# Performance work log

Measured on AMD Instinct MI355X. Metric: run time of the kernel, lower is better.

Reference implementation:

```python
import jax, jax.numpy as jnp
import numpy as np

NEG_SLOPE = 0.2  # negative_slope of LeakyReLU in GATConv
N_NODES = 50000
N_EDGES = 800000
R = 2
IN_DIM = 128
HID = 32
HEADS = 4
OUT = 32


def setup_inputs() -> dict:
    key = jax.random.key(0)
    ks = jax.random.split(key, 12)
    s = 0.1  # keep pre-activations tame
    x = jax.random.normal(ks[0], (N_NODES, IN_DIM), dtype=jnp.float32)
    W1 = jax.random.normal(ks[1], (R, IN_DIM, HEADS * HID), dtype=jnp.float32) * s
    al1 = jax.random.normal(ks[2], (R, HEADS, HID), dtype=jnp.float32) * s
    ar1 = jax.random.normal(ks[3], (R, HEADS, HID), dtype=jnp.float32) * s
    b1 = jax.random.normal(ks[4], (R, HEADS * HID), dtype=jnp.float32) * s
    W2 = jax.random.normal(ks[5], (R, HEADS * HID, HEADS * OUT), dtype=jnp.float32) * s
    al2 = jax.random.normal(ks[6], (R, HEADS, OUT), dtype=jnp.float32) * s
    ar2 = jax.random.normal(ks[7], (R, HEADS, OUT), dtype=jnp.float32) * s
    b2 = jax.random.normal(ks[8], (R, HEADS * OUT), dtype=jnp.float32) * s
    edges = jax.random.randint(ks[9], (R, 2, N_EDGES), 0, N_NODES, dtype=jnp.int32)
    return {"x": x, "W1": W1, "al1": al1, "ar1": ar1, "b1": b1,
            "W2": W2, "al2": al2, "ar2": ar2, "b2": b2, "edges": edges}


def _gat_rel(h, W, al, ar, src, dst, n):
    """Single-relation GATConv aggregation (no bias/residual/activation)."""
    H, D = al.shape
    feat = (h @ W).reshape(n, H, D)                   # [N,H,D]
    el = jnp.einsum('nhd,hd->nh', feat, al)           # [N,H]
    er = jnp.einsum('nhd,hd->nh', feat, ar)
    e = el[src] + er[dst]                             # [E,H]
    e = jnp.where(e > 0, e, NEG_SLOPE * e)            # LeakyReLU
    # edge softmax over incoming edges of each dst node (numerically stable)
    m = jax.ops.segment_max(e, dst, num_segments=n)
    ex = jnp.exp(e - m[dst])
    denom = jax.ops.segment_sum(ex, dst, num_segments=n)
    alpha = ex / jnp.maximum(denom[dst], 1e-9)        # [E,H]
    msg = alpha[:, :, None] * feat[src]               # [E,H,D]
    return jax.ops.segment_sum(msg, dst, num_segments=n)  # [N,H,D]


def reference(x, W1, al1, ar1, b1, W2, al2, ar2, b2, edges):
    n = x.shape[0]
    r_count = edges.shape[0]
    H1, D1 = al1.shape[1:]
    # --- layer 1: per-relation GATConv (bias + elu inside), sum across relations
    acc = jnp.zeros((n, H1, D1), dtype=x.dtype)
    for r in range(r_count):
        src, dst = edges[r, 0], edges[r, 1]
        o = _gat_rel(x, W1[r], al1[r], ar1[r], src, dst, n)
        acc = acc + jax.nn.elu(o + b1[r].reshape(1, H1, D1))
    h = acc.reshape(n, H1 * D1)                       # flatten heads
    # --- layer 2: residual (identity, since in == heads*out), bias, no activation
    H2, D2 = al2.shape[1:]
    res = h.reshape(n, H2, D2)
    acc2 = jnp.zeros((n, H2, D2), dtype=x.dtype)
    for r in range(r_count):
        src, dst = edges[r, 0], edges[r, 1]
        o = _gat_rel(h, W2[r], al2[r], ar2[r], src, dst, n)
        acc2 = acc2 + o + res + b2[r].reshape(1, H2, D2)
    return acc2.mean(axis=1)                          # mean over heads -> [N, OUT]
```

## Files before the change

### kernel.cpp

```cpp
#include <hip/hip_runtime.h>
#include <math.h>

#define HEADS 4
#define DIM 32
#define FDIM 128
#define EPB 8192
#define BPBSH 8
#define WB 16

typedef __attribute__((ext_vector_type(8))) short short8;
typedef __attribute__((ext_vector_type(16))) float float16;

__device__ __forceinline__ unsigned short f2bf(float x) {
  unsigned u = __float_as_uint(x);
  u += 0x7FFFu + ((u >> 16) & 1);
  return (unsigned short)(u >> 16);
}

__global__ __launch_bounds__(256) void binA_kernel(const int* __restrict__ edges,
    int* __restrict__ cntA, const float* __restrict__ W1, const float* __restrict__ W2,
    unsigned short* __restrict__ WT, int E, int BA, int BAp, int R) {
  int r = blockIdx.y, blk = blockIdx.x, t = threadIdx.x;
  if (blk >= BA) {
    int wb = blk - BA;
    int base = wb * (32768 / WB);
#pragma unroll
    for (int j = 0; j < 32768 / WB; j += 256) {
      int idx = base + j + t;
      int layer = idx >> 14;
      int rem = idx & 16383;
      int n = rem >> 7, k = rem & 127;
      const float* W = layer ? (W2 + (size_t)r * FDIM * FDIM)
                             : (W1 + (size_t)r * FDIM * FDIM);
      WT[((size_t)(layer * R + r) << 14) + rem] = f2bf(W[k * FDIM + n]);
    }
    return;
  }
  __shared__ int hist[256];
  hist[t] = 0;
  __syncthreads();
  const int* dst = edges + (size_t)r * 2 * E + E;
  int base = blk * EPB;
#pragma unroll
  for (int j = 0; j < EPB / 256; ++j) {
    int e = base + t + j * 256;
    if (e < E) atomicAdd(&hist[dst[e] >> BPBSH], 1);
  }
  __syncthreads();
  cntA[((size_t)r * 256 + t) * BAp + blk] = hist[t];
}

__global__ __launch_bounds__(256) void scanP1_kernel(const int* __restrict__ cntA,
    int* __restrict__ btot, int BA, int BAp) {
  int r = blockIdx.y, b = blockIdx.x, t = threadIdx.x;
  const int* row = cntA + ((size_t)r * 256 + b) * BAp;
  int v = 0;
  for (int i = t; i < BA; i += 256) v += row[i];
  __shared__ int s[256];
  s[t] = v;
  __syncthreads();
  for (int ofs = 128; ofs > 0; ofs >>= 1) {
    if (t < ofs) s[t] += s[t + ofs];
    __syncthreads();
  }
  if (t == 0) btot[r * 256 + b] = s[0];
}

__global__ __launch_bounds__(256) void scanP2_kernel(int* __restrict__ btot,
    int* __restrict__ bucketBase, int E, int NB) {
  __shared__ int s[256];
  int r = blockIdx.x, b = threadIdx.x;
  int v = btot[r * 256 + b];
  s[b] = v;
  __syncthreads();
  for (int ofs = 1; ofs < 256; ofs <<= 1) {
    int u = (b >= ofs) ? s[b - ofs] : 0;
    __syncthreads();
    s[b] += u;
    __syncthreads();
  }
  int excl = s[b] - v;
  if (b < NB) bucketBase[r * 257 + b] = excl;
  if (b == 0) bucketBase[r * 257 + NB] = E;
  btot[r * 256 + b] = excl;
}

__global__ __launch_bounds__(256) void scanP3_kernel(int* __restrict__ cntA,
    const int* __restrict__ bexcl, int BA, int BAp) {
  int r = blockIdx.y, b = blockIdx.x, t = threadIdx.x;
  int* row = cntA + ((size_t)r * 256 + b) * BAp;
  __shared__ int s[256];
  int carry = bexcl[r * 256 + b];
  for (int base0 = 0; base0 < BA; base0 += 256) {
    int idx = base0 + t;
    int v = (idx < BA) ? row[idx] : 0;
    s[t] = v;
    __syncthreads();
    for (int ofs = 1; ofs < 256; ofs <<= 1) {
      int u = (t >= ofs) ? s[t - ofs] : 0;
      __syncthreads();
      s[t] += u;
      __syncthreads();
    }
    int excl = s[t] - v;
    if (idx < BA) row[idx] = carry + excl;
    int tot = s[255];
    __syncthreads();
    carry += tot;
  }
}

__global__ __launch_bounds__(256) void scatterA_kernel(const int* __restrict__ edges,
    const int* __restrict__ cntA, unsigned* __restrict__ binned, int E, int BA, int BAp) {
  __shared__ int cur[256];
  int r = blockIdx.y, blk = blockIdx.x, t = threadIdx.x;
  cur[t] = cntA[((size_t)r * 256 + t) * BAp + blk];
  __syncthreads();
  const int* srcp = edges + (size_t)r * 2 * E;
  const int* dstp = srcp + E;
  unsigned* bout = binned + (size_t)r * E;
  int base = blk * EPB;
#pragma unroll
  for (int j = 0; j < EPB / 256; ++j) {
    int e = base + t + j * 256;
    if (e < E) {
      int d = dstp[e], s = srcp[e];
      int pos = atomicAdd(&cur[d >> BPBSH], 1);
      bout[pos] = ((unsigned)d << 16) | (unsigned)s;
    }
  }
}

__global__ __launch_bounds__(256) void passB_kernel(const unsigned* __restrict__ binned,
    const int* __restrict__ bucketBase, unsigned short* __restrict__ csr,
    int* __restrict__ indptr, int E, int N, int NB) {
  __shared__ int cnt[256];
  __shared__ int off[256];
  __shared__ int cur[256];
  int r = blockIdx.y, b = blockIdx.x, t = threadIdx.x;
  int beg = bucketBase[r * 257 + b];
  int end = bucketBase[r * 257 + b + 1];
  cnt[t] = 0;
  __syncthreads();
  const unsigned* bin = binned + (size_t)r * E;
  for (int i = beg + t; i < end; i += 256)
    atomicAdd(&cnt[(bin[i] >> 16) & 255], 1);
  __syncthreads();
  for (int ofs = 1; ofs < 256; ofs <<= 1) {
    int u = (t >= ofs) ? cnt[t - ofs] : 0;
    __syncthreads();
    cnt[t] += u;
    __syncthreads();
  }
  int ex = beg + ((t > 0) ? cnt[t - 1] : 0);
  off[t] = ex;
  cur[t] = ex;
  __syncthreads();
  int node = b * 256 + t;
  if (node < N) indptr[(size_t)r * (N + 1) + node] = off[t];
  if (b == NB - 1 && t == 0) indptr[(size_t)r * (N + 1) + N] = E;
  unsigned short* csr_r = csr + (size_t)r * E;
  for (int i = beg + t; i < end; i += 256) {
    unsigned p = bin[i];
    int rank = atomicAdd(&cur[(p >> 16) & 255], 1);
    csr_r[rank] = (unsigned short)(p & 0xFFFFu);
  }
}

__global__ __launch_bounds__(256) void mm_kernel(const float* __restrict__ A,
    const unsigned short* __restrict__ WTl, const float* __restrict__ al_all,
    const float* __restrict__ ar_all, unsigned short* __restrict__ featb_all,
    float* __restrict__ el_all, float* __restrict__ er_all, int N) {
  __shared__ unsigned short sA[128 * 136];
  __shared__ float sAl[FDIM], sAr[FDIM];
  int r = blockIdx.y;
  const unsigned short* WT = WTl + (size_t)r * FDIM * FDIM;
  int row0 = blockIdx.x * 128;
  int t = threadIdx.x;
  if (t < FDIM) {
    sAl[t] = al_all[r * FDIM + t];
    sAr[t] = ar_all[r * FDIM + t];
  }
#pragma unroll
  for (int it = 0; it < 16; ++it) {
    int idx = t * 4 + it * 1024;
    int row = idx >> 7, k = idx & 127;
    int grow = row0 + row;
    float4 v = make_float4(0.f, 0.f, 0.f, 0.f);
    if (grow < N) v = *(const float4*)(A + (size_t)grow * FDIM + k);
    unsigned short* p = sA + row * 136 + k;
    p[0] = f2bf(v.x); p[1] = f2bf(v.y); p[2] = f2bf(v.z); p[3] = f2bf(v.w);
  }
  __syncthreads();
  int lane = t & 63, w = t >> 6;
  int m = lane & 31, q = lane >> 5;
  float16 acc[4] = {0.f, 0.f, 0.f, 0.f};
#pragma unroll
  for (int kc = 0; kc < 8; ++kc) {
    int ko = kc * 16 + q * 8;
    short8 a = *(const short8*)(sA + (w * 32 + m) * 136 + ko);
#pragma unroll
    for (int nt = 0; nt < 4; ++nt) {
      short8 bb = *(const short8*)(WT + (size_t)(nt * 32 + m) * FDIM + ko);
      acc[nt] = __builtin_amdgcn_mfma_f32_32x32x16_bf16(a, bb, acc[nt], 0, 0, 0);
    }
  }
  __syncthreads();
#pragma unroll
  for (int nt = 0; nt < 4; ++nt) {
#pragma unroll
    for (int reg = 0; reg < 16; ++reg) {
      int rr = (reg & 3) + 8 * (reg >> 2) + 4 * q;
      sA[(w * 32 + rr) * 136 + nt * 32 + m] = f2bf(acc[nt][reg]);
    }
  }
  __syncthreads();
  unsigned short* fb = featb_all + (size_t)r * N * FDIM;
#pragma unroll
  for (int it = 0; it < 8; ++it) {
    int idx = (t + it * 256) * 8;
    int row = idx >> 7, k = idx & 127;
    int grow = row0 + row;
    if (grow < N)
      *(uint4*)(fb + (size_t)grow * FDIM + k) = *(const uint4*)(sA + row * 136 + k);
  }
  int rowc = t >> 1, grow = row0 + rowc;
  if (grow < N) {
    float* elr = el_all + (size_t)r * N * 4;
    float* err_ = er_all + (size_t)r * N * 4;
#pragma unroll
    for (int hh = 0; hh < 2; ++hh) {
      int hd = (t & 1) * 2 + hh;
      const uint4* rp4 = (const uint4*)(sA + rowc * 136 + hd * DIM);
      const float4* alp = (const float4*)(sAl + hd * DIM);
      const float4* arp = (const float4*)(sAr + hd * DIM);
      float sl = 0.f, sr = 0.f;
#pragma unroll
      for (int gq = 0; gq < 4; ++gq) {
        uint4 u = rp4[gq];
        float4 a0 = alp[2 * gq], a1 = alp[2 * gq + 1];
        float4 r0 = arp[2 * gq], r1 = arp[2 * gq + 1];
        unsigned uv[4] = {u.x, u.y, u.z, u.w};
        float fv[8];
#pragma unroll
        for (int j = 0; j < 4; ++j) {
          fv[2 * j] = __uint_as_float(uv[j] << 16);
          fv[2 * j + 1] = __uint_as_float(uv[j] & 0xFFFF0000u);
        }
        sl = fmaf(fv[0], a0.x, sl); sr = fmaf(fv[0], r0.x, sr);
        sl = fmaf(fv[1], a0.y, sl); sr = fmaf(fv[1], r0.y, sr);
        sl = fmaf(fv[2], a0.z, sl); sr = fmaf(fv[2], r0.z, sr);
        sl = fmaf(fv[3], a0.w, sl); sr = fmaf(fv[3], r0.w, sr);
        sl = fmaf(fv[4], a1.x, sl); sr = fmaf(fv[4], r1.x, sr);
        sl = fmaf(fv[5], a1.y, sl); sr = fmaf(fv[5], r1.y, sr);
        sl = fmaf(fv[6], a1.z, sl); sr = fmaf(fv[6], r1.z, sr);
        sl = fmaf(fv[7], a1.w, sl); sr = fmaf(fv[7], r1.w, sr);
      }
      elr[(size_t)grow * 4 + hd] = sl;
      err_[(size_t)grow * 4 + hd] = sr;
    }
  }
}

__global__ __launch_bounds__(256) void agg1_kernel(const unsigned short* __restrict__ featb,
    const float* __restrict__ el, const float* __restrict__ er,
    const int* __restrict__ indptr, const unsigned short* __restrict__ csr,
    const float* __restrict__ bias, float* __restrict__ hout, int N, int E, int R) {
  int t = blockIdx.x * 256 + threadIdx.x;
  int node = t >> 3;
  if (node >= N) return;
  int hd = t & 3, sub = (t >> 2) & 1;
  float tot[32];
#pragma unroll
  for (int i = 0; i < 32; ++i) tot[i] = 0.f;
  for (int r = 0; r < R; ++r) {
    const unsigned short* f = featb + (size_t)r * N * FDIM + hd * DIM;
    const float* elr = el + (size_t)r * N * 4;
    const unsigned short* csr_r = csr + (size_t)r * E;
    const int* ip = indptr + (size_t)r * (N + 1);
    float er_h = er[(size_t)r * N * 4 + node * 4 + hd];
    int beg = ip[node], end = ip[node + 1];
    float l = 0.f, a[32];
#pragma unroll
    for (int i = 0; i < 32; ++i) a[i] = 0.f;
    for (int i = beg + sub; i < end; i += 2) {
      int s = csr_r[i];
      float ee = elr[s * 4 + hd] + er_h;
      ee = ee > 0.f ? ee : 0.2f * ee;
      float p = __expf(ee);
      const uint4* fp = (const uint4*)(f + (size_t)s * FDIM);
      uint4 u0 = fp[0], u1 = fp[1], u2 = fp[2], u3 = fp[3];
      l += p;
      unsigned uu[16] = {u0.x, u0.y, u0.z, u0.w, u1.x, u1.y, u1.z, u1.w,
                         u2.x, u2.y, u2.z, u2.w, u3.x, u3.y, u3.z, u3.w};
#pragma unroll
      for (int j = 0; j < 16; ++j) {
        float f0 = __uint_as_float(uu[j] << 16);
        float f1 = __uint_as_float(uu[j] & 0xFFFF0000u);
        a[2 * j]     = fmaf(p, f0, a[2 * j]);
        a[2 * j + 1] = fmaf(p, f1, a[2 * j + 1]);
      }
    }
    l += __shfl_xor(l, 4);
#pragma unroll
    for (int i = 0; i < 32; ++i) a[i] += __shfl_xor(a[i], 4);
    float inv = (l > 0.f) ? 1.f / l : 0.f;
    const float4* b4 = (const float4*)(bias + r * FDIM + hd * DIM);
#pragma unroll
    for (int g = 0; g < 8; ++g) {
      float4 bv = b4[g];
      float v0 = a[4 * g] * inv + bv.x;
      float v1 = a[4 * g + 1] * inv + bv.y;
      float v2 = a[4 * g + 2] * inv + bv.z;
      float v3 = a[4 * g + 3] * inv + bv.w;
      tot[4 * g]     += v0 > 0.f ? v0 : __expf(v0) - 1.f;
      tot[4 * g + 1] += v1 > 0.f ? v1 : __expf(v1) - 1.f;
      tot[4 * g + 2] += v2 > 0.f ? v2 : __expf(v2) - 1.f;
      tot[4 * g + 3] += v3 > 0.f ? v3 : __expf(v3) - 1.f;
    }
  }
  if (sub == 0) {
    float4* hp = (float4*)(hout + (size_t)node * FDIM + hd * DIM);
#pragma unroll
    for (int g = 0; g < 8; ++g)
      hp[g] = make_float4(tot[4 * g], tot[4 * g + 1], tot[4 * g + 2], tot[4 * g + 3]);
  }
}

__global__ __launch_bounds__(256) void agg2_kernel(const unsigned short* __restrict__ featb,
    const float* __restrict__ el, const float* __restrict__ er,
    const int* __restrict__ indptr, const unsigned short* __restrict__ csr,
    const float* __restrict__ bias, const float* __restrict__ hf,
    float* __restrict__ out, int N, int E, int R) {
  int t = blockIdx.x * 256 + threadIdx.x;
  int node = t >> 3;
  if (node >= N) return;
  int hd = t & 3, sub = (t >> 2) & 1;
  float tot[32];
#pragma unroll
  for (int i = 0; i < 32; ++i) tot[i] = 0.f;
  for (int r = 0; r < R; ++r) {
    const unsigned short* f = featb + (size_t)r * N * FDIM + hd * DIM;
    const float* elr = el + (size_t)r * N * 4;
    const unsigned short* csr_r = csr + (size_t)r * E;
    const int* ip = indptr + (size_t)r * (N + 1);
    float er_h = er[(size_t)r * N * 4 + node * 4 + hd];
    int beg = ip[node], end = ip[node + 1];
    float l = 0.f, a[32];
#pragma unroll
    for (int i = 0; i < 32; ++i) a[i] = 0.f;
    for (int i = beg + sub; i < end; i += 2) {
      int s = csr_r[i];
      float ee = elr[s * 4 + hd] + er_h;
      ee = ee > 0.f ? ee : 0.2f * ee;
      float p = __expf(ee);
      const uint4* fp = (const uint4*)(f + (size_t)s * FDIM);
      uint4 u0 = fp[0], u1 = fp[1], u2 = fp[2], u3 = fp[3];
      l += p;
      unsigned uu[16] = {u0.x, u0.y, u0.z, u0.w, u1.x, u1.y, u1.z, u1.w,
                         u2.x, u2.y, u2.z, u2.w, u3.x, u3.y, u3.z, u3.w};
#pragma unroll
      for (int j = 0; j < 16; ++j) {
        float f0 = __uint_as_float(uu[j] << 16);
        float f1 = __uint_as_float(uu[j] & 0xFFFF0000u);
        a[2 * j]     = fmaf(p, f0, a[2 * j]);
        a[2 * j + 1] = fmaf(p, f1, a[2 * j + 1]);
      }
    }
    l += __shfl_xor(l, 4);
#pragma unroll
    for (int i = 0; i < 32; ++i) a[i] += __shfl_xor(a[i], 4);
    float inv = (l > 0.f) ? 1.f / l : 0.f;
    const float4* b4 = (const float4*)(bias + r * FDIM + hd * DIM);
#pragma unroll
    for (int g = 0; g < 8; ++g) {
      float4 bv = b4[g];
      tot[4 * g]     += a[4 * g] * inv + bv.x;
      tot[4 * g + 1] += a[4 * g + 1] * inv + bv.y;
      tot[4 * g + 2] += a[4 * g + 2] * inv + bv.z;
      tot[4 * g + 3] += a[4 * g + 3] * inv + bv.w;
    }
  }
  {
    const float4* rv4 = (const float4*)(hf + (size_t)node * FDIM + hd * DIM);
#pragma unroll
    for (int g = 0; g < 8; ++g) {
      float4 rv = rv4[g];
      tot[4 * g]     += R * rv.x;
      tot[4 * g + 1] += R * rv.y;
      tot[4 * g + 2] += R * rv.z;
      tot[4 * g + 3] += R * rv.w;
    }
  }
#pragma unroll
  for (int i = 0; i < 32; ++i) {
    float v = tot[i];
    v += __shfl_xor(v, 1);
    v += __shfl_xor(v, 2);
    tot[i] = v * 0.25f;
  }
  if (sub == 0) {
    float4* op = (float4*)(out + (size_t)node * 32 + hd * 8);
    op[0] = make_float4(tot[hd * 8], tot[hd * 8 + 1], tot[hd * 8 + 2], tot[hd * 8 + 3]);
    op[1] = make_float4(tot[hd * 8 + 4], tot[hd * 8 + 5], tot[hd * 8 + 6], tot[hd * 8 + 7]);
  }
}

extern "C" void kernel_launch(void* const* d_in, const int* in_sizes, int n_in,
                              void* d_out, int out_size, void* d_ws, size_t ws_size,
                              hipStream_t stream) {
  const float* x   = (const float*)d_in[0];
  const float* W1  = (const float*)d_in[1];
  const float* al1 = (const float*)d_in[2];
  const float* ar1 = (const float*)d_in[3];
  const float* b1  = (const float*)d_in[4];
  const float* W2  = (const float*)d_in[5];
  const float* al2 = (const float*)d_in[6];
  const float* ar2 = (const float*)d_in[7];
  const float* b2  = (const float*)d_in[8];
  const int* edges = (const int*)d_in[9];
  float* out = (float*)d_out;

  const int N = in_sizes[0] / FDIM;
  const int R = in_sizes[1] / (FDIM * FDIM);
  const int E = in_sizes[9] / (2 * R);
  const int BA = (E + EPB - 1) / EPB;
  const int BAp = (BA + 3) & ~3;
  const int NB = (N + 255) >> BPBSH;

  char* ws = (char*)d_ws;
  size_t off = 0;
  auto alloc = [&](size_t bytes) {
    char* p = ws + off;
    off += (bytes + 255) & ~(size_t)255;
    return p;
  };
  unsigned short* featb = (unsigned short*)alloc((size_t)R * N * FDIM * 2);
  unsigned short* WT    = (unsigned short*)alloc((size_t)2 * R * FDIM * FDIM * 2);
  float* el = (float*)alloc((size_t)R * N * 4 * 4);
  float* er = (float*)alloc((size_t)R * N * 4 * 4);
  float* h  = (float*)alloc((size_t)N * FDIM * 4);
  int* cntA = (int*)alloc((size_t)R * 256 * BAp * 4);
  int* bucketBase = (int*)alloc((size_t)R * 257 * 4);
  int* btot = (int*)alloc((size_t)R * 256 * 4);
  unsigned* binned = (unsigned*)alloc((size_t)R * E * 4);
  unsigned short* csr = (unsigned short*)alloc((size_t)R * E * 2);
  int* indptr = (int*)alloc((size_t)R * (N + 1) * 4);

  dim3 bgrid(BA + WB, R);
  binA_kernel<<<bgrid, 256, 0, stream>>>(edges, cntA, W1, W2, WT, E, BA, BAp, R);
  dim3 pgrid256(256, R);
  scanP1_kernel<<<pgrid256, 256, 0, stream>>>(cntA, btot, BA, BAp);
  scanP2_kernel<<<R, 256, 0, stream>>>(btot, bucketBase, E, NB);
  scanP3_kernel<<<pgrid256, 256, 0, stream>>>(cntA, btot, BA, BAp);
  dim3 sgrid(BA, R);
  scatterA_kernel<<<sgrid, 256, 0, stream>>>(edges, cntA, binned, E, BA, BAp);
  dim3 pgrid(NB, R);
  passB_kernel<<<pgrid, 256, 0, stream>>>(binned, bucketBase, csr, indptr, E, N, NB);

  dim3 mmgrid((N + 127) / 128, R);
  int agrid = (N * 8 + 255) / 256;

  mm_kernel<<<mmgrid, 256, 0, stream>>>(x, WT, al1, ar1, featb, el, er, N);
  agg1_kernel<<<agrid, 256, 0, stream>>>(featb, el, er, indptr, csr, b1, h, N, E, R);

  mm_kernel<<<mmgrid, 256, 0, stream>>>(h, WT + (size_t)R * FDIM * FDIM, al2, ar2, featb, el, er, N);
  agg2_kernel<<<agrid, 256, 0, stream>>>(featb, el, er, indptr, csr, b2, h, out, N, E, R);
}
```

Before: 347.0 us.

## Software-pipeline neighbor gathers in aggregation and fuse scan phases two and three

The aggregation loops in both GAT layers now issue the next neighbor's feature and logit loads before accumulating the current edge, so memory latency overlaps with the FMA work. Separately, the small per-relation scan of bucket totals is folded into the third scan kernel: each block recomputes the 256-entry prefix itself, which removes one kernel launch at the cost of some redundant work. The prefetch holds extra registers for the next edge's data, which may lower occupancy.

```diff
diff --git a/kernel.cpp b/kernel.cpp
--- a/kernel.cpp
+++ b/kernel.cpp
@@ -66,35 +66,30 @@
   if (t == 0) btot[r * 256 + b] = s[0];
 }
 
-__global__ __launch_bounds__(256) void scanP2_kernel(int* __restrict__ btot,
-    int* __restrict__ bucketBase, int E, int NB) {
+__global__ __launch_bounds__(256) void scanP3_kernel(int* __restrict__ cntA,
+    const int* __restrict__ btot, int* __restrict__ bucketBase,
+    int E, int NB, int BA, int BAp) {
+  int r = blockIdx.y, b = blockIdx.x, t = threadIdx.x;
   __shared__ int s[256];
-  int r = blockIdx.x, b = threadIdx.x;
-  int v = btot[r * 256 + b];
-  s[b] = v;
+  int v = btot[r * 256 + t];
+  s[t] = v;
   __syncthreads();
   for (int ofs = 1; ofs < 256; ofs <<= 1) {
-    int u = (b >= ofs) ? s[b - ofs] : 0;
-    __syncthreads();
-    s[b] += u;
-    __syncthreads();
-  }
-  int excl = s[b] - v;
-  if (b < NB) bucketBase[r * 257 + b] = excl;
-  if (b == 0) bucketBase[r * 257 + NB] = E;
-  btot[r * 256 + b] = excl;
-}
-
-__global__ __launch_bounds__(256) void scanP3_kernel(int* __restrict__ cntA,
-    const int* __restrict__ bexcl, int BA, int BAp) {
-  int r = blockIdx.y, b = blockIdx.x, t = threadIdx.x;
+    int u = (t >= ofs) ? s[t - ofs] : 0;
+    __syncthreads();
+    s[t] += u;
+    __syncthreads();
+  }
+  int vb = btot[r * 256 + b];
+  int carry = s[b] - vb;
+  if (t == b && b < NB) bucketBase[r * 257 + b] = carry;
+  if (b == 0 && t == 0) bucketBase[r * 257 + NB] = E;
+  __syncthreads();
   int* row = cntA + ((size_t)r * 256 + b) * BAp;
-  __shared__ int s[256];
-  int carry = bexcl[r * 256 + b];
   for (int base0 = 0; base0 < BA; base0 += 256) {
     int idx = base0 + t;
-    int v = (idx < BA) ? row[idx] : 0;
-    s[t] = v;
+    int w = (idx < BA) ? row[idx] : 0;
+    s[t] = w;
     __syncthreads();
     for (int ofs = 1; ofs < 256; ofs <<= 1) {
       int u = (t >= ofs) ? s[t - ofs] : 0;
@@ -102,7 +97,7 @@
       s[t] += u;
       __syncthreads();
     }
-    int excl = s[t] - v;
+    int excl = s[t] - w;
     if (idx < BA) row[idx] = carry + excl;
     int tot = s[255];
     __syncthreads();
@@ -262,6 +257,19 @@
   }
 }
 
+__device__ __forceinline__ void acc_edge(float (&a)[32], uint4 u0, uint4 u1,
+                                         uint4 u2, uint4 u3, float p) {
+  unsigned uu[16] = {u0.x, u0.y, u0.z, u0.w, u1.x, u1.y, u1.z, u1.w,
+                     u2.x, u2.y, u2.z, u2.w, u3.x, u3.y, u3.z, u3.w};
+#pragma unroll
+  for (int j = 0; j < 16; ++j) {
+    float f0 = __uint_as_float(uu[j] << 16);
+    float f1 = __uint_as_float(uu[j] & 0xFFFF0000u);
+    a[2 * j]     = fmaf(p, f0, a[2 * j]);
+    a[2 * j + 1] = fmaf(p, f1, a[2 * j + 1]);
+  }
+}
+
 __global__ __launch_bounds__(256) void agg1_kernel(const unsigned short* __restrict__ featb,
     const float* __restrict__ el, const float* __restrict__ er,
     const int* __restrict__ indptr, const unsigned short* __restrict__ csr,
@@ -283,27 +291,33 @@
     float l = 0.f, a[32];
 #pragma unroll
     for (int i = 0; i < 32; ++i) a[i] = 0.f;
-    for (int i = beg + sub; i < end; i += 2) {
+    int i = beg + sub;
+    if (i < end) {
       int s = csr_r[i];
-      float ee = elr[s * 4 + hd] + er_h;
+      const uint4* fp = (const uint4*)(f + (size_t)s * FDIM);
+      uint4 c0 = fp[0], c1 = fp[1], c2 = fp[2], c3 = fp[3];
+      float ec = elr[s * 4 + hd];
+      for (i += 2; i < end; i += 2) {
+        int s2 = csr_r[i];
+        const uint4* fq = (const uint4*)(f + (size_t)s2 * FDIM);
+        uint4 n0 = fq[0], n1 = fq[1], n2 = fq[2], n3 = fq[3];
+        float en = elr[s2 * 4 + hd];
+        float ee = ec + er_h;
+        ee = ee > 0.f ? ee : 0.2f * ee;
+        float p = __expf(ee);
+        l += p;
+        acc_edge(a, c0, c1, c2, c3, p);
+        c0 = n0; c1 = n1; c2 = n2; c3 = n3; ec = en;
+      }
+      float ee = ec + er_h;
       ee = ee > 0.f ? ee : 0.2f * ee;
       float p = __expf(ee);
-      const uint4* fp = (const uint4*)(f + (size_t)s * FDIM);
-      uint4 u0 = fp[0], u1 = fp[1], u2 = fp[2], u3 = fp[3];
       l += p;
-      unsigned uu[16] = {u0.x, u0.y, u0.z, u0.w, u1.x, u1.y, u1.z, u1.w,
-                         u2.x, u2.y, u2.z, u2.w, u3.x, u3.y, u3.z, u3.w};
-#pragma unroll
-      for (int j = 0; j < 16; ++j) {
-        float f0 = __uint_as_float(uu[j] << 16);
-        float f1 = __uint_as_float(uu[j] & 0xFFFF0000u);
-        a[2 * j]     = fmaf(p, f0, a[2 * j]);
-        a[2 * j + 1] = fmaf(p, f1, a[2 * j + 1]);
-      }
+      acc_edge(a, c0, c1, c2, c3, p);
     }
     l += __shfl_xor(l, 4);
 #pragma unroll
-    for (int i = 0; i < 32; ++i) a[i] += __shfl_xor(a[i], 4);
+    for (int i2 = 0; i2 < 32; ++i2) a[i2] += __shfl_xor(a[i2], 4);
     float inv = (l > 0.f) ? 1.f / l : 0.f;
     const float4* b4 = (const float4*)(bias + r * FDIM + hd * DIM);
 #pragma unroll
@@ -349,27 +363,33 @@
     float l = 0.f, a[32];
 #pragma unroll
     for (int i = 0; i < 32; ++i) a[i] = 0.f;
-    for (int i = beg + sub; i < end; i += 2) {
+    int i = beg + sub;
+    if (i < end) {
       int s = csr_r[i];
-      float ee = elr[s * 4 + hd] + er_h;
+      const uint4* fp = (const uint4*)(f + (size_t)s * FDIM);
+      uint4 c0 = fp[0], c1 = fp[1], c2 = fp[2], c3 = fp[3];
+      float ec = elr[s * 4 + hd];
+      for (i += 2; i < end; i += 2) {
+        int s2 = csr_r[i];
+        const uint4* fq = (const uint4*)(f + (size_t)s2 * FDIM);
+        uint4 n0 = fq[0], n1 = fq[1], n2 = fq[2], n3 = fq[3];
+        float en = elr[s2 * 4 + hd];
+        float ee = ec + er_h;
+        ee = ee > 0.f ? ee : 0.2f * ee;
+        float p = __expf(ee);
+        l += p;
+        acc_edge(a, c0, c1, c2, c3, p);
+        c0 = n0; c1 = n1; c2 = n2; c3 = n3; ec = en;
+      }
+      float ee = ec + er_h;
       ee = ee > 0.f ? ee : 0.2f * ee;
       float p = __expf(ee);
-      const uint4* fp = (const uint4*)(f + (size_t)s * FDIM);
-      uint4 u0 = fp[0], u1 = fp[1], u2 = fp[2], u3 = fp[3];
       l += p;
-      unsigned uu[16] = {u0.x, u0.y, u0.z, u0.w, u1.x, u1.y, u1.z, u1.w,
-                         u2.x, u2.y, u2.z, u2.w, u3.x, u3.y, u3.z, u3.w};
-#pragma unroll
-      for (int j = 0; j < 16; ++j) {
-        float f0 = __uint_as_float(uu[j] << 16);
-        float f1 = __uint_as_float(uu[j] & 0xFFFF0000u);
-        a[2 * j]     = fmaf(p, f0, a[2 * j]);
-        a[2 * j + 1] = fmaf(p, f1, a[2 * j + 1]);
-      }
+      acc_edge(a, c0, c1, c2, c3, p);
     }
     l += __shfl_xor(l, 4);
 #pragma unroll
-    for (int i = 0; i < 32; ++i) a[i] += __shfl_xor(a[i], 4);
+    for (int i2 = 0; i2 < 32; ++i2) a[i2] += __shfl_xor(a[i2], 4);
     float inv = (l > 0.f) ? 1.f / l : 0.f;
     const float4* b4 = (const float4*)(bias + r * FDIM + hd * DIM);
 #pragma unroll
@@ -451,8 +471,7 @@
   binA_kernel<<<bgrid, 256, 0, stream>>>(edges, cntA, W1, W2, WT, E, BA, BAp, R);
   dim3 pgrid256(256, R);
   scanP1_kernel<<<pgrid256, 256, 0, stream>>>(cntA, btot, BA, BAp);
-  scanP2_kernel<<<R, 256, 0, stream>>>(btot, bucketBase, E, NB);
-  scanP3_kernel<<<pgrid256, 256, 0, stream>>>(cntA, btot, BA, BAp);
+  scanP3_kernel<<<pgrid256, 256, 0, stream>>>(cntA, btot, bucketBase, E, NB, BA, BAp);
   dim3 sgrid(BA, R);
   scatterA_kernel<<<sgrid, 256, 0, stream>>>(edges, cntA, binned, E, BA, BAp);
   dim3 pgrid(NB, R);
```

Result: slower. 363.9 us (+4.9%).
